# Kernel optimization log

Measured on AMD Instinct MI355X. Metric: run time of the kernel, lower is better.

The kernel has to match this reference:

```python
import jax, jax.numpy as jnp
import numpy as np

NODES = 8192
RANK = 10  # hardcoded inner dim in the original module


def setup_inputs() -> dict:
    key = jax.random.key(0)
    k1, k2 = jax.random.split(key)
    nodevec1 = jax.random.normal(k1, (NODES, RANK), dtype=jnp.float32)
    nodevec2 = jax.random.normal(k2, (RANK, NODES), dtype=jnp.float32)
    return {"nodevec1": nodevec1, "nodevec2": nodevec2}


def reference(nodevec1, nodevec2):
    # [N, 10] @ [10, N] -> [N, N]; relu; row softmax (dim=1)
    scores = jax.nn.relu(jnp.matmul(nodevec1, nodevec2))
    return jax.nn.softmax(scores, axis=1)
```

## Files before the change

kernel.cpp:

```cpp
#include <hip/hip_runtime.h>


#define NODES 8192
#define RANK  10
#define TPB   1024
#define NWAVE (TPB / 64)
#define ROWS_PER_BLOCK 32
#define NBLOCKS (NODES / ROWS_PER_BLOCK)
#define BATCH 2

__global__ __launch_bounds__(TPB)
void fused_gsoftmax_kernel(const float* __restrict__ nv1,
                           const float* __restrict__ nv2,
                           float* __restrict__ out)
{
    const int t    = threadIdx.x;
    const int lane = t & 63;
    const int wave = t >> 6;
    const int row0 = blockIdx.x * ROWS_PER_BLOCK;

    float4 b[2][RANK];
#pragma unroll
    for (int g = 0; g < 2; ++g) {
        const int j = g * 4096 + t * 4;
#pragma unroll
        for (int k = 0; k < RANK; ++k)
            b[g][k] = *reinterpret_cast<const float4*>(nv2 + k * NODES + j);
    }

    __shared__ float red[NWAVE][BATCH];

    for (int rb = 0; rb < ROWS_PER_BLOCK; rb += BATCH) {
        float e[BATCH][2][4];
        float psum[BATCH];

#pragma unroll
        for (int r = 0; r < BATCH; ++r) {
            const int row = row0 + rb + r;
            float a[RANK];
#pragma unroll
            for (int k = 0; k < RANK; ++k) a[k] = nv1[row * RANK + k];

            float sum = 0.0f;
#pragma unroll
            for (int g = 0; g < 2; ++g) {
                float4 acc = make_float4(0.f, 0.f, 0.f, 0.f);
#pragma unroll
                for (int k = 0; k < RANK; ++k) {
                    acc.x = fmaf(a[k], b[g][k].x, acc.x);
                    acc.y = fmaf(a[k], b[g][k].y, acc.y);
                    acc.z = fmaf(a[k], b[g][k].z, acc.z);
                    acc.w = fmaf(a[k], b[g][k].w, acc.w);
                }
                e[r][g][0] = __expf(fmaxf(acc.x, 0.f));
                e[r][g][1] = __expf(fmaxf(acc.y, 0.f));
                e[r][g][2] = __expf(fmaxf(acc.z, 0.f));
                e[r][g][3] = __expf(fmaxf(acc.w, 0.f));
                sum += ((e[r][g][0] + e[r][g][1]) + (e[r][g][2] + e[r][g][3]));
            }
            psum[r] = sum;
        }

#pragma unroll
        for (int r = 0; r < BATCH; ++r)
#pragma unroll
            for (int m = 32; m >= 1; m >>= 1)
                psum[r] += __shfl_xor(psum[r], m, 64);
        if (lane == 0) {
#pragma unroll
            for (int r = 0; r < BATCH; ++r) red[wave][r] = psum[r];
        }
        __syncthreads();

        float inv[BATCH];
#pragma unroll
        for (int r = 0; r < BATCH; ++r) {
            float s = 0.0f;
#pragma unroll
            for (int w = 0; w < NWAVE; ++w) s += red[w][r];
            inv[r] = 1.0f / s;
        }
        __syncthreads();

#pragma unroll
        for (int r = 0; r < BATCH; ++r) {
            const int row = row0 + rb + r;
            float* __restrict__ orow = out + (size_t)row * NODES;
#pragma unroll
            for (int g = 0; g < 2; ++g) {
                const int j = g * 4096 + t * 4;
                float4 o;
                o.x = e[r][g][0] * inv[r];
                o.y = e[r][g][1] * inv[r];
                o.z = e[r][g][2] * inv[r];
                o.w = e[r][g][3] * inv[r];
                *reinterpret_cast<float4*>(orow + j) = o;
            }
        }
    }
}

extern "C" void kernel_launch(void* const* d_in, const int* in_sizes, int n_in,
                              void* d_out, int out_size, void* d_ws, size_t ws_size,
                              hipStream_t stream)
{
    const float* nv1 = (const float*)d_in[0];
    const float* nv2 = (const float*)d_in[1];
    float* out = (float*)d_out;

    fused_gsoftmax_kernel<<<NBLOCKS, TPB, 0, stream>>>(nv1, nv2, out);
}
```

Measured before the change: 296.5 us.

## Split fused softmax into row-sum pass and sync-free recompute-and-store pass

Replaces the single fused kernel, which synchronized the block twice per pair of rows, with two kernels. The first computes per-row exp sums for 32 rows with one block barrier and writes reciprocals to workspace. The second recomputes the rank-10 dot products and exps, scales them, and writes the output with nontemporal stores and no barriers. The intent is to keep the 256 MB output write stream free of synchronization stalls, at the cost of doing the compute and exps twice and an extra kernel launch.

```diff
diff --git a/kernel.cpp b/kernel.cpp
--- a/kernel.cpp
+++ b/kernel.cpp
@@ -5,19 +5,21 @@
 #define RANK  10
 #define TPB   1024
 #define NWAVE (TPB / 64)
-#define ROWS_PER_BLOCK 32
-#define NBLOCKS (NODES / ROWS_PER_BLOCK)
-#define BATCH 2
+#define RPB   32
+#define NBLK  (NODES / RPB)
+#define CHUNK 8
+
+typedef float f32x4 __attribute__((ext_vector_type(4)));
 
 __global__ __launch_bounds__(TPB)
-void fused_gsoftmax_kernel(const float* __restrict__ nv1,
-                           const float* __restrict__ nv2,
-                           float* __restrict__ out)
+void rowsum_kernel(const float* __restrict__ nv1,
+                   const float* __restrict__ nv2,
+                   float* __restrict__ rowinv)
 {
     const int t    = threadIdx.x;
     const int lane = t & 63;
     const int wave = t >> 6;
-    const int row0 = blockIdx.x * ROWS_PER_BLOCK;
+    const int row0 = blockIdx.x * RPB;
 
     float4 b[2][RANK];
 #pragma unroll
@@ -28,15 +30,13 @@
             b[g][k] = *reinterpret_cast<const float4*>(nv2 + k * NODES + j);
     }
 
-    __shared__ float red[NWAVE][BATCH];
+    __shared__ float red[NWAVE][RPB];
 
-    for (int rb = 0; rb < ROWS_PER_BLOCK; rb += BATCH) {
-        float e[BATCH][2][4];
-        float psum[BATCH];
-
+    for (int c = 0; c < RPB; c += CHUNK) {
+        float psum[CHUNK];
 #pragma unroll
-        for (int r = 0; r < BATCH; ++r) {
-            const int row = row0 + rb + r;
+        for (int r = 0; r < CHUNK; ++r) {
+            const int row = row0 + c + r;
             float a[RANK];
 #pragma unroll
             for (int k = 0; k < RANK; ++k) a[k] = nv1[row * RANK + k];
@@ -52,50 +52,76 @@
                     acc.z = fmaf(a[k], b[g][k].z, acc.z);
                     acc.w = fmaf(a[k], b[g][k].w, acc.w);
                 }
-                e[r][g][0] = __expf(fmaxf(acc.x, 0.f));
-                e[r][g][1] = __expf(fmaxf(acc.y, 0.f));
-                e[r][g][2] = __expf(fmaxf(acc.z, 0.f));
-                e[r][g][3] = __expf(fmaxf(acc.w, 0.f));
-                sum += ((e[r][g][0] + e[r][g][1]) + (e[r][g][2] + e[r][g][3]));
+                sum += __expf(fmaxf(acc.x, 0.f)) + __expf(fmaxf(acc.y, 0.f))
+                     + __expf(fmaxf(acc.z, 0.f)) + __expf(fmaxf(acc.w, 0.f));
             }
             psum[r] = sum;
         }
-
 #pragma unroll
-        for (int r = 0; r < BATCH; ++r)
+        for (int r = 0; r < CHUNK; ++r) {
 #pragma unroll
             for (int m = 32; m >= 1; m >>= 1)
                 psum[r] += __shfl_xor(psum[r], m, 64);
+        }
         if (lane == 0) {
 #pragma unroll
-            for (int r = 0; r < BATCH; ++r) red[wave][r] = psum[r];
+            for (int r = 0; r < CHUNK; ++r) red[wave][c + r] = psum[r];
         }
-        __syncthreads();
+    }
 
-        float inv[BATCH];
+    __syncthreads();
+    if (t < RPB) {
+        float s = 0.0f;
 #pragma unroll
-        for (int r = 0; r < BATCH; ++r) {
-            float s = 0.0f;
+        for (int w = 0; w < NWAVE; ++w) s += red[w][t];
+        rowinv[row0 + t] = 1.0f / s;
+    }
+}
+
+__global__ __launch_bounds__(TPB)
+void stream_kernel(const float* __restrict__ nv1,
+                   const float* __restrict__ nv2,
+                   const float* __restrict__ rowinv,
+                   float* __restrict__ out)
+{
+    const int t    = threadIdx.x;
+    const int row0 = blockIdx.x * RPB;
+
+    float4 b[2][RANK];
 #pragma unroll
-            for (int w = 0; w < NWAVE; ++w) s += red[w][r];
-            inv[r] = 1.0f / s;
-        }
-        __syncthreads();
+    for (int g = 0; g < 2; ++g) {
+        const int j = g * 4096 + t * 4;
+#pragma unroll
+        for (int k = 0; k < RANK; ++k)
+            b[g][k] = *reinterpret_cast<const float4*>(nv2 + k * NODES + j);
+    }
 
+#pragma unroll 2
+    for (int r = 0; r < RPB; ++r) {
+        const int row = row0 + r;
+        const float inv = rowinv[row];
+        float a[RANK];
 #pragma unroll
-        for (int r = 0; r < BATCH; ++r) {
-            const int row = row0 + rb + r;
-            float* __restrict__ orow = out + (size_t)row * NODES;
+        for (int k = 0; k < RANK; ++k) a[k] = nv1[row * RANK + k];
+
+        float* __restrict__ orow = out + (size_t)row * NODES;
 #pragma unroll
-            for (int g = 0; g < 2; ++g) {
-                const int j = g * 4096 + t * 4;
-                float4 o;
-                o.x = e[r][g][0] * inv[r];
-                o.y = e[r][g][1] * inv[r];
-                o.z = e[r][g][2] * inv[r];
-                o.w = e[r][g][3] * inv[r];
-                *reinterpret_cast<float4*>(orow + j) = o;
+        for (int g = 0; g < 2; ++g) {
+            const int j = g * 4096 + t * 4;
+            float4 acc = make_float4(0.f, 0.f, 0.f, 0.f);
+#pragma unroll
+            for (int k = 0; k < RANK; ++k) {
+                acc.x = fmaf(a[k], b[g][k].x, acc.x);
+                acc.y = fmaf(a[k], b[g][k].y, acc.y);
+                acc.z = fmaf(a[k], b[g][k].z, acc.z);
+                acc.w = fmaf(a[k], b[g][k].w, acc.w);
             }
+            f32x4 o;
+            o.x = __expf(fmaxf(acc.x, 0.f)) * inv;
+            o.y = __expf(fmaxf(acc.y, 0.f)) * inv;
+            o.z = __expf(fmaxf(acc.z, 0.f)) * inv;
+            o.w = __expf(fmaxf(acc.w, 0.f)) * inv;
+            __builtin_nontemporal_store(o, reinterpret_cast<f32x4*>(orow + j));
         }
     }
 }
@@ -106,7 +132,9 @@
 {
     const float* nv1 = (const float*)d_in[0];
     const float* nv2 = (const float*)d_in[1];
-    float* out = (float*)d_out;
+    float* out    = (float*)d_out;
+    float* rowinv = (float*)d_ws;
 
-    fused_gsoftmax_kernel<<<NBLOCKS, TPB, 0, stream>>>(nv1, nv2, out);
+    rowsum_kernel<<<NBLK, TPB, 0, stream>>>(nv1, nv2, rowinv);
+    stream_kernel<<<NBLK, TPB, 0, stream>>>(nv1, nv2, rowinv, out);
 }
```

Result: no change. 299.9 us (+1.1%).
